# Kernel optimization log

Measured on AMD Instinct MI355X. Metric: run time of the kernel, lower is better.

## Reference

```python
import jax, jax.numpy as jnp
import numpy as np

N_NODES = 100000
N_EDGES = 3200000
D_FEAT = 128


def setup_inputs() -> dict:
    key = jax.random.key(0)
    k1, k2, k3, k4 = jax.random.split(key, 4)
    edge_row = jax.random.randint(k1, (N_EDGES,), 0, N_NODES, dtype=jnp.int64 if jax.config.jax_enable_x64 else jnp.int32)
    edge_col = jax.random.randint(k2, (N_EDGES,), 0, N_NODES, dtype=edge_row.dtype)
    edge_val = jax.random.uniform(k3, (N_EDGES,), dtype=jnp.float32)
    embeds = jax.random.normal(k4, (N_NODES, D_FEAT), dtype=jnp.float32)
    return {"edge_row": edge_row, "edge_col": edge_col, "edge_val": edge_val, "embeds": embeds}


def reference(edge_row, edge_col, edge_val, embeds):
    # SpMM: out[r] = sum_{e: row(e)=r} val(e) * embeds[col(e)]
    messages = edge_val[:, None] * embeds[edge_col]  # [E, D]
    out = jax.ops.segment_sum(messages, edge_row, num_segments=embeds.shape[0])  # [N, D]
    return out
```

## Files before the change

kernel.cpp:

```cpp
#include <hip/hip_runtime.h>
#include <stdint.h>

#define N_NODES 100000
#define D_FEAT  128
#define RSH     6
#define RPB     64
#define NBUCK   ((N_NODES + RPB - 1) / RPB)
#define CAPF    2304
#define KMAX    ((CAPF + 255) / 256)
#define OCAP    8192
#define SC_THR  1024
#define SC_EPT  8
#define SC_TILE (SC_THR * SC_EPT)
#define COLMASK 0x1FFFF

__global__ __launch_bounds__(SC_THR) void scatter_fixed_kernel(
    const int* __restrict__ row, const int* __restrict__ col,
    const float* __restrict__ val, int* __restrict__ cursor,
    int2* __restrict__ rec, int4* __restrict__ oflow, int* __restrict__ ocnt, int n,
    const uint64_t* __restrict__ embin, uint32_t* __restrict__ embbf, int do_conv)
{
    __shared__ int cnt[NBUCK];
    __shared__ int base[NBUCK];
    const int tid = threadIdx.x;

    if (do_conv) {
        const int n2 = N_NODES * (D_FEAT / 2);
        const int stride = (int)gridDim.x * SC_THR;
        for (int i = (int)blockIdx.x * SC_THR + tid; i < n2; i += stride) {
            uint64_t u = __builtin_nontemporal_load(embin + i);
            uint32_t bx = (uint32_t)u, by = (uint32_t)(u >> 32);
            bx = (bx + 0x7FFFu + ((bx >> 16) & 1u)) >> 16;
            by = (by + 0x7FFFu + ((by >> 16) & 1u)) >> 16;
            embbf[i] = bx | (by << 16);
        }
    }

    const int e0 = (int)blockIdx.x * SC_TILE + tid * SC_EPT;

    for (int i = tid; i < NBUCK; i += SC_THR) cnt[i] = 0;
    __syncthreads();

    int   r[SC_EPT], c[SC_EPT];
    float v[SC_EPT];
    if (e0 + SC_EPT <= n) {
        const int4* rp = (const int4*)(row + e0);
        const int4* cp = (const int4*)(col + e0);
        const float4* vp = (const float4*)(val + e0);
        #pragma unroll
        for (int q = 0; q < SC_EPT / 4; q++) {
            int4 rr = rp[q]; int4 cc = cp[q]; float4 vv = vp[q];
            r[q*4+0]=rr.x; r[q*4+1]=rr.y; r[q*4+2]=rr.z; r[q*4+3]=rr.w;
            c[q*4+0]=cc.x; c[q*4+1]=cc.y; c[q*4+2]=cc.z; c[q*4+3]=cc.w;
            v[q*4+0]=vv.x; v[q*4+1]=vv.y; v[q*4+2]=vv.z; v[q*4+3]=vv.w;
        }
    } else {
        #pragma unroll
        for (int k = 0; k < SC_EPT; k++) {
            int e = e0 + k;
            if (e < n) { r[k] = row[e]; c[k] = col[e]; v[k] = val[e]; }
            else       { r[k] = -1; }
        }
    }

    int rk[SC_EPT];
    #pragma unroll
    for (int k = 0; k < SC_EPT; k++)
        if (r[k] >= 0) rk[k] = atomicAdd(&cnt[r[k] >> RSH], 1);
    __syncthreads();

    for (int i = tid; i < NBUCK; i += SC_THR) {
        int cc = cnt[i];
        if (cc) base[i] = atomicAdd(&cursor[i], cc);
    }
    __syncthreads();

    #pragma unroll
    for (int k = 0; k < SC_EPT; k++) {
        if (r[k] >= 0) {
            int bk  = r[k] >> RSH;
            int pos = base[bk] + rk[k];
            if (pos < CAPF) {
                rec[(size_t)bk * CAPF + pos] =
                    make_int2(((r[k] & (RPB - 1)) << 17) | c[k], __float_as_int(v[k]));
            } else {
                int op = atomicAdd(ocnt, 1);
                if (op < OCAP) oflow[op] = make_int4(r[k], c[k], __float_as_int(v[k]), 0);
            }
        }
    }
}

template <bool BF16>
__global__ __launch_bounds__(256) void spmm_fixed_kernel(const int* __restrict__ fill,
                                                         const int2* __restrict__ rec,
                                                         const void* __restrict__ emb,
                                                         float* __restrict__ out)
{
    __shared__ int2 buf[CAPF];
    __shared__ int  cnt[RPB];
    __shared__ int  start[RPB];
    __shared__ int  sc_[RPB];

    const int tid  = threadIdx.x;
    const int lane = tid & 63;
    const int wv   = tid >> 6;
    const int b    = blockIdx.x;
    const int m    = min(fill[b], CAPF);
    const uint64_t* __restrict__ rec8 = (const uint64_t*)rec + (size_t)b * CAPF;
    const uint32_t* __restrict__ embu = (const uint32_t*)emb;
    const float2*   __restrict__ emb2 = (const float2*)emb;

    if (tid < RPB) cnt[tid] = 0;
    __syncthreads();

    int2 rc[KMAX];
    int  rk[KMAX];
    #pragma unroll
    for (int k = 0; k < KMAX; k++) {
        int i = k * 256 + tid;
        if (i < m) {
            uint64_t u = __builtin_nontemporal_load(rec8 + i);
            rc[k].x = (int)(uint32_t)u;
            rc[k].y = (int)(uint32_t)(u >> 32);
            rk[k] = atomicAdd(&cnt[(uint32_t)rc[k].x >> 17], 1);
        }
    }
    __syncthreads();
    if (tid < RPB) sc_[tid] = cnt[tid];
    __syncthreads();
    for (int off = 1; off < RPB; off <<= 1) {
        int t = 0;
        if (tid < RPB && tid >= off) t = sc_[tid - off];
        __syncthreads();
        if (tid < RPB) sc_[tid] += t;
        __syncthreads();
    }
    if (tid < RPB) start[tid] = sc_[tid] - cnt[tid];
    __syncthreads();
    #pragma unroll
    for (int k = 0; k < KMAX; k++) {
        int i = k * 256 + tid;
        if (i < m) buf[start[(uint32_t)rc[k].x >> 17] + rk[k]] = rc[k];
    }
    __syncthreads();

    for (int rl = wv * 16; rl < wv * 16 + 16; rl++) {
        const int s0 = start[rl];
        const int c0 = cnt[rl];
        float ax = 0.f, ay = 0.f;
        int j = 0;
        for (; j + 16 <= c0; j += 16) {
            uint32_t u[16]; float vv[16]; float2 m2[16];
            #pragma unroll
            for (int q = 0; q < 16; q++) {
                int2 e = buf[s0 + j + q];
                uint32_t off = (((uint32_t)e.x & COLMASK) << 6) | (uint32_t)lane;
                vv[q] = __int_as_float(e.y);
                if (BF16) u[q] = embu[off]; else m2[q] = emb2[off];
            }
            #pragma unroll
            for (int q = 0; q < 16; q++) {
                if (BF16) {
                    ax += vv[q] * __uint_as_float(u[q] << 16);
                    ay += vv[q] * __uint_as_float(u[q] & 0xFFFF0000u);
                } else {
                    ax += vv[q] * m2[q].x; ay += vv[q] * m2[q].y;
                }
            }
        }
        for (; j + 4 <= c0; j += 4) {
            uint32_t u[4]; float vv[4]; float2 m2[4];
            #pragma unroll
            for (int q = 0; q < 4; q++) {
                int2 e = buf[s0 + j + q];
                uint32_t off = (((uint32_t)e.x & COLMASK) << 6) | (uint32_t)lane;
                vv[q] = __int_as_float(e.y);
                if (BF16) u[q] = embu[off]; else m2[q] = emb2[off];
            }
            #pragma unroll
            for (int q = 0; q < 4; q++) {
                if (BF16) {
                    ax += vv[q] * __uint_as_float(u[q] << 16);
                    ay += vv[q] * __uint_as_float(u[q] & 0xFFFF0000u);
                } else {
                    ax += vv[q] * m2[q].x; ay += vv[q] * m2[q].y;
                }
            }
        }
        for (; j < c0; j++) {
            int2 e = buf[s0 + j];
            uint32_t off = (((uint32_t)e.x & COLMASK) << 6) | (uint32_t)lane;
            float vv = __int_as_float(e.y);
            if (BF16) {
                uint32_t u = embu[off];
                ax += vv * __uint_as_float(u << 16);
                ay += vv * __uint_as_float(u & 0xFFFF0000u);
            } else {
                float2 mm = emb2[off];
                ax += vv * mm.x; ay += vv * mm.y;
            }
        }
        const int grow = b * RPB + rl;
        if (grow < N_NODES) {
            uint64_t w = (uint64_t)__float_as_uint(ax) | ((uint64_t)__float_as_uint(ay) << 32);
            __builtin_nontemporal_store(w, (uint64_t*)out + (size_t)grow * 64 + lane);
        }
    }
}

__global__ __launch_bounds__(256) void oflow_kernel(const int4* __restrict__ oflow,
                                                    const int* __restrict__ ocnt,
                                                    const float* __restrict__ embeds,
                                                    float* __restrict__ out) {
    const int nof  = min(*ocnt, OCAP);
    const int lane = threadIdx.x & 63;
    const int w    = ((int)blockIdx.x * 256 + threadIdx.x) >> 6;
    const int nw   = ((int)gridDim.x * 256) >> 6;
    for (int i = w; i < nof; i += nw) {
        int4 e = oflow[i];
        const float2* src = (const float2*)(embeds + (size_t)e.y * D_FEAT);
        float2 mm = src[lane];
        float vv = __int_as_float(e.z);
        float* dst = out + (size_t)e.x * D_FEAT + (lane << 1);
        unsafeAtomicAdd(dst,     vv * mm.x);
        unsafeAtomicAdd(dst + 1, vv * mm.y);
    }
}

__global__ __launch_bounds__(256) void spmm_atomic_kernel(
    const int* __restrict__ edge_row, const int* __restrict__ edge_col,
    const float* __restrict__ edge_val, const float* __restrict__ embeds,
    float* __restrict__ out, int n_edges)
{
    const int lane    = threadIdx.x & 63;
    const int wave_id = ((int)blockIdx.x * blockDim.x + threadIdx.x) >> 6;
    const int n_waves = ((int)gridDim.x * blockDim.x) >> 6;
    for (int e = wave_id; e < n_edges; e += n_waves) {
        const int   r = edge_row[e];
        const int   c = edge_col[e];
        const float vv = edge_val[e];
        const float2* src = (const float2*)(embeds + (size_t)c * D_FEAT);
        float2 mm = src[lane];
        float* dst = out + (size_t)r * D_FEAT + (lane << 1);
        unsafeAtomicAdd(dst,     vv * mm.x);
        unsafeAtomicAdd(dst + 1, vv * mm.y);
    }
}

static inline size_t align256(size_t x) { return (x + 255) & ~(size_t)255; }

extern "C" void kernel_launch(void* const* d_in, const int* in_sizes, int n_in,
                              void* d_out, int out_size, void* d_ws, size_t ws_size,
                              hipStream_t stream) {
    const int*   edge_row = (const int*)d_in[0];
    const int*   edge_col = (const int*)d_in[1];
    const float* edge_val = (const float*)d_in[2];
    const float* embeds   = (const float*)d_in[3];
    float*       out      = (float*)d_out;

    const int n_edges = in_sizes[0];

    size_t off = 0;
    size_t o_cursor = off; off = align256(off + (size_t)(NBUCK + 1) * 4);
    size_t o_oflow  = off; off = align256(off + (size_t)OCAP * 16);
    size_t o_rec    = off; off = align256(off + (size_t)NBUCK * CAPF * 8);
    const size_t need_fp32 = off;
    size_t o_emb    = off; off = align256(off + (size_t)N_NODES * 64 * 4);
    const size_t need_bf16 = off;

    if (ws_size < need_fp32) {
        hipMemsetAsync(out, 0, (size_t)out_size * sizeof(float), stream);
        spmm_atomic_kernel<<<dim3(4096), dim3(256), 0, stream>>>(
            edge_row, edge_col, edge_val, embeds, out, n_edges);
        return;
    }

    char* ws = (char*)d_ws;
    int*      cursor = (int*)(ws + o_cursor);
    int*      ocnt   = cursor + NBUCK;
    int4*     oflow  = (int4*)(ws + o_oflow);
    int2*     rec    = (int2*)(ws + o_rec);
    uint32_t* embbf  = (uint32_t*)(ws + o_emb);

    const bool use_bf16 = (ws_size >= need_bf16);

    hipMemsetAsync(cursor, 0, (size_t)(NBUCK + 1) * 4, stream);
    scatter_fixed_kernel<<<dim3((n_edges + SC_TILE - 1) / SC_TILE), dim3(SC_THR), 0, stream>>>(
        edge_row, edge_col, edge_val, cursor, rec, oflow, ocnt, n_edges,
        (const uint64_t*)embeds, embbf, use_bf16 ? 1 : 0);
    if (use_bf16)
        spmm_fixed_kernel<true><<<dim3(NBUCK), dim3(256), 0, stream>>>(cursor, rec, embbf, out);
    else
        spmm_fixed_kernel<false><<<dim3(NBUCK), dim3(256), 0, stream>>>(cursor, rec, embeds, out);
    oflow_kernel<<<dim3(16), dim3(256), 0, stream>>>(oflow, ocnt, embeds, out);
}
```

Measured before the change: 275.4 us.

## Split each SpMM bucket across four blocks and batch gather loads

The SpMM kernel now launches four blocks per 64-row bucket. Each block re-reads the whole bucket's records but keeps only the 16 rows it owns, so each wave handles 4 rows instead of 16. This raises the number of blocks and waves in flight for better latency hiding, and adds launch_bounds occupancy hints and sched_barriers that group the 16 gather loads together. The cost is four times the record reads from global memory plus the extra local sorting work.

```diff
diff --git a/kernel.cpp b/kernel.cpp
--- a/kernel.cpp
+++ b/kernel.cpp
@@ -8,6 +8,7 @@
 #define NBUCK   ((N_NODES + RPB - 1) / RPB)
 #define CAPF    2304
 #define KMAX    ((CAPF + 255) / 256)
+#define QROWS   16
 #define OCAP    8192
 #define SC_THR  1024
 #define SC_EPT  8
@@ -92,26 +93,27 @@
 }
 
 template <bool BF16>
-__global__ __launch_bounds__(256) void spmm_fixed_kernel(const int* __restrict__ fill,
-                                                         const int2* __restrict__ rec,
-                                                         const void* __restrict__ emb,
-                                                         float* __restrict__ out)
+__global__ __launch_bounds__(256, 8) void spmm_fixed_kernel(const int* __restrict__ fill,
+                                                            const int2* __restrict__ rec,
+                                                            const void* __restrict__ emb,
+                                                            float* __restrict__ out)
 {
     __shared__ int2 buf[CAPF];
-    __shared__ int  cnt[RPB];
-    __shared__ int  start[RPB];
-    __shared__ int  sc_[RPB];
+    __shared__ int  cnt[QROWS];
+    __shared__ int  start[QROWS];
+    __shared__ int  sc_[QROWS];
 
     const int tid  = threadIdx.x;
     const int lane = tid & 63;
     const int wv   = tid >> 6;
-    const int b    = blockIdx.x;
+    const int b    = blockIdx.x >> 2;
+    const int qq   = blockIdx.x & 3;
     const int m    = min(fill[b], CAPF);
     const uint64_t* __restrict__ rec8 = (const uint64_t*)rec + (size_t)b * CAPF;
     const uint32_t* __restrict__ embu = (const uint32_t*)emb;
     const float2*   __restrict__ emb2 = (const float2*)emb;
 
-    if (tid < RPB) cnt[tid] = 0;
+    if (tid < QROWS) cnt[tid] = 0;
     __syncthreads();
 
     int2 rc[KMAX];
@@ -119,33 +121,36 @@
     #pragma unroll
     for (int k = 0; k < KMAX; k++) {
         int i = k * 256 + tid;
+        rk[k] = -1;
         if (i < m) {
             uint64_t u = __builtin_nontemporal_load(rec8 + i);
             rc[k].x = (int)(uint32_t)u;
             rc[k].y = (int)(uint32_t)(u >> 32);
-            rk[k] = atomicAdd(&cnt[(uint32_t)rc[k].x >> 17], 1);
-        }
-    }
-    __syncthreads();
-    if (tid < RPB) sc_[tid] = cnt[tid];
-    __syncthreads();
-    for (int off = 1; off < RPB; off <<= 1) {
+            int rl = (int)((uint32_t)rc[k].x >> 17);
+            if ((rl >> 4) == qq)
+                rk[k] = atomicAdd(&cnt[rl & (QROWS - 1)], 1);
+        }
+    }
+    __syncthreads();
+    if (tid < QROWS) sc_[tid] = cnt[tid];
+    __syncthreads();
+    for (int off = 1; off < QROWS; off <<= 1) {
         int t = 0;
-        if (tid < RPB && tid >= off) t = sc_[tid - off];
+        if (tid < QROWS && tid >= off) t = sc_[tid - off];
         __syncthreads();
-        if (tid < RPB) sc_[tid] += t;
+        if (tid < QROWS) sc_[tid] += t;
         __syncthreads();
     }
-    if (tid < RPB) start[tid] = sc_[tid] - cnt[tid];
+    if (tid < QROWS) start[tid] = sc_[tid] - cnt[tid];
     __syncthreads();
     #pragma unroll
     for (int k = 0; k < KMAX; k++) {
-        int i = k * 256 + tid;
-        if (i < m) buf[start[(uint32_t)rc[k].x >> 17] + rk[k]] = rc[k];
-    }
-    __syncthreads();
-
-    for (int rl = wv * 16; rl < wv * 16 + 16; rl++) {
+        if (rk[k] >= 0)
+            buf[start[((uint32_t)rc[k].x >> 17) & (QROWS - 1)] + rk[k]] = rc[k];
+    }
+    __syncthreads();
+
+    for (int rl = wv * 4; rl < wv * 4 + 4; rl++) {
         const int s0 = start[rl];
         const int c0 = cnt[rl];
         float ax = 0.f, ay = 0.f;
@@ -155,10 +160,16 @@
             #pragma unroll
             for (int q = 0; q < 16; q++) {
                 int2 e = buf[s0 + j + q];
-                uint32_t off = (((uint32_t)e.x & COLMASK) << 6) | (uint32_t)lane;
+                u[q]  = (((uint32_t)e.x & COLMASK) << 6) | (uint32_t)lane;
                 vv[q] = __int_as_float(e.y);
-                if (BF16) u[q] = embu[off]; else m2[q] = emb2[off];
-            }
+            }
+            __builtin_amdgcn_sched_barrier(0);
+            #pragma unroll
+            for (int q = 0; q < 16; q++) {
+                if (BF16) u[q] = embu[u[q]];
+                else      m2[q] = emb2[u[q]];
+            }
+            __builtin_amdgcn_sched_barrier(0);
             #pragma unroll
             for (int q = 0; q < 16; q++) {
                 if (BF16) {
@@ -174,9 +185,12 @@
             #pragma unroll
             for (int q = 0; q < 4; q++) {
                 int2 e = buf[s0 + j + q];
-                uint32_t off = (((uint32_t)e.x & COLMASK) << 6) | (uint32_t)lane;
+                u[q]  = (((uint32_t)e.x & COLMASK) << 6) | (uint32_t)lane;
                 vv[q] = __int_as_float(e.y);
-                if (BF16) u[q] = embu[off]; else m2[q] = emb2[off];
+            }
+            #pragma unroll
+            for (int q = 0; q < 4; q++) {
+                if (BF16) u[q] = embu[u[q]]; else m2[q] = emb2[u[q]];
             }
             #pragma unroll
             for (int q = 0; q < 4; q++) {
@@ -201,7 +215,7 @@
                 ax += vv * mm.x; ay += vv * mm.y;
             }
         }
-        const int grow = b * RPB + rl;
+        const int grow = b * RPB + qq * QROWS + rl;
         if (grow < N_NODES) {
             uint64_t w = (uint64_t)__float_as_uint(ax) | ((uint64_t)__float_as_uint(ay) << 32);
             __builtin_nontemporal_store(w, (uint64_t*)out + (size_t)grow * 64 + lane);
@@ -290,8 +304,8 @@
         edge_row, edge_col, edge_val, cursor, rec, oflow, ocnt, n_edges,
         (const uint64_t*)embeds, embbf, use_bf16 ? 1 : 0);
     if (use_bf16)
-        spmm_fixed_kernel<true><<<dim3(NBUCK), dim3(256), 0, stream>>>(cursor, rec, embbf, out);
+        spmm_fixed_kernel<true><<<dim3(NBUCK * 4), dim3(256), 0, stream>>>(cursor, rec, embbf, out);
     else
-        spmm_fixed_kernel<false><<<dim3(NBUCK), dim3(256), 0, stream>>>(cursor, rec, embeds, out);
+        spmm_fixed_kernel<false><<<dim3(NBUCK * 4), dim3(256), 0, stream>>>(cursor, rec, embeds, out);
     oflow_kernel<<<dim3(16), dim3(256), 0, stream>>>(oflow, ocnt, embeds, out);
 }
```

Result: no change. 280.1 us (+1.7%).

## Sort block edges by column slab then row to localize embedding gathers

Applied to the files above, without the earlier changes.

Within each row-bucket block, edges are now counting-sorted by a composite key of column slab (col>>13) and local row, so the block walks all rows one column slab at a time. Each wave keeps 16 row accumulators in registers and handles row pairs with up to 12 outstanding gathers. The aim is temporal locality across concurrent blocks in L2/MALL for the embedding table, plus more gathers in flight. The cost is a larger shared-memory prefix scan over 832 keys, more registers (launch_bounds hints 5 blocks/CU), and per-pair divergence overhead when there are few edges per key.

```diff
diff --git a/kernel.cpp b/kernel.cpp
--- a/kernel.cpp
+++ b/kernel.cpp
@@ -8,6 +8,8 @@
 #define NBUCK   ((N_NODES + RPB - 1) / RPB)
 #define CAPF    2304
 #define KMAX    ((CAPF + 255) / 256)
+#define NSH     13
+#define KEYS    (NSH * RPB)
 #define OCAP    8192
 #define SC_THR  1024
 #define SC_EPT  8
@@ -92,15 +94,15 @@
 }
 
 template <bool BF16>
-__global__ __launch_bounds__(256) void spmm_fixed_kernel(const int* __restrict__ fill,
-                                                         const int2* __restrict__ rec,
-                                                         const void* __restrict__ emb,
-                                                         float* __restrict__ out)
+__global__ __launch_bounds__(256, 5) void spmm_fixed_kernel(const int* __restrict__ fill,
+                                                            const int2* __restrict__ rec,
+                                                            const void* __restrict__ emb,
+                                                            float* __restrict__ out)
 {
     __shared__ int2 buf[CAPF];
-    __shared__ int  cnt[RPB];
-    __shared__ int  start[RPB];
-    __shared__ int  sc_[RPB];
+    __shared__ int  cnt[KEYS];
+    __shared__ int  start[KEYS];
+    __shared__ int  sc_[KEYS];
 
     const int tid  = threadIdx.x;
     const int lane = tid & 63;
@@ -111,99 +113,119 @@
     const uint32_t* __restrict__ embu = (const uint32_t*)emb;
     const float2*   __restrict__ emb2 = (const float2*)emb;
 
-    if (tid < RPB) cnt[tid] = 0;
+    for (int i = tid; i < KEYS; i += 256) cnt[i] = 0;
     __syncthreads();
 
     int2 rc[KMAX];
     int  rk[KMAX];
+    int  ky[KMAX];
     #pragma unroll
     for (int k = 0; k < KMAX; k++) {
         int i = k * 256 + tid;
+        rk[k] = -1;
         if (i < m) {
             uint64_t u = __builtin_nontemporal_load(rec8 + i);
             rc[k].x = (int)(uint32_t)u;
             rc[k].y = (int)(uint32_t)(u >> 32);
-            rk[k] = atomicAdd(&cnt[(uint32_t)rc[k].x >> 17], 1);
-        }
-    }
-    __syncthreads();
-    if (tid < RPB) sc_[tid] = cnt[tid];
-    __syncthreads();
-    for (int off = 1; off < RPB; off <<= 1) {
-        int t = 0;
-        if (tid < RPB && tid >= off) t = sc_[tid - off];
+            uint32_t col = (uint32_t)rc[k].x & COLMASK;
+            uint32_t rl  = (uint32_t)rc[k].x >> 17;
+            ky[k] = (int)((col >> 13) * RPB + rl);
+            rk[k] = atomicAdd(&cnt[ky[k]], 1);
+        }
+    }
+    __syncthreads();
+
+    for (int i = tid; i < KEYS; i += 256) sc_[i] = cnt[i];
+    __syncthreads();
+    for (int off = 1; off < KEYS; off <<= 1) {
+        int t[4];
+        #pragma unroll
+        for (int z = 0; z < 4; z++) {
+            int i = tid + z * 256;
+            t[z] = (i < KEYS && i >= off) ? sc_[i - off] : 0;
+        }
         __syncthreads();
-        if (tid < RPB) sc_[tid] += t;
+        #pragma unroll
+        for (int z = 0; z < 4; z++) {
+            int i = tid + z * 256;
+            if (i < KEYS) sc_[i] += t[z];
+        }
         __syncthreads();
     }
-    if (tid < RPB) start[tid] = sc_[tid] - cnt[tid];
-    __syncthreads();
-    #pragma unroll
-    for (int k = 0; k < KMAX; k++) {
-        int i = k * 256 + tid;
-        if (i < m) buf[start[(uint32_t)rc[k].x >> 17] + rk[k]] = rc[k];
-    }
-    __syncthreads();
-
-    for (int rl = wv * 16; rl < wv * 16 + 16; rl++) {
-        const int s0 = start[rl];
-        const int c0 = cnt[rl];
-        float ax = 0.f, ay = 0.f;
-        int j = 0;
-        for (; j + 16 <= c0; j += 16) {
-            uint32_t u[16]; float vv[16]; float2 m2[16];
+    for (int i = tid; i < KEYS; i += 256) start[i] = sc_[i] - cnt[i];
+    __syncthreads();
+
+    #pragma unroll
+    for (int k = 0; k < KMAX; k++)
+        if (rk[k] >= 0) buf[start[ky[k]] + rk[k]] = rc[k];
+    __syncthreads();
+
+    float ax[16], ay[16];
+    #pragma unroll
+    for (int p = 0; p < 16; p++) { ax[p] = 0.f; ay[p] = 0.f; }
+
+    for (int s = 0; s < NSH; s++) {
+        const int kbase = s * RPB + wv * 16;
+        #pragma unroll
+        for (int p = 0; p < 8; p++) {
+            const int ka = kbase + 2 * p;
+            const int ca = cnt[ka], cb = cnt[ka + 1];
+            const int nfull = __builtin_amdgcn_readfirstlane(ca + cb);
+            if (nfull == 0) continue;
+            const int ss = __builtin_amdgcn_readfirstlane(ca);
+            const int sa = start[ka];
+            const int nn = nfull < 12 ? nfull : 12;
+
+            uint32_t u[12]; float vv[12]; float2 m2[12];
             #pragma unroll
-            for (int q = 0; q < 16; q++) {
-                int2 e = buf[s0 + j + q];
+            for (int q = 0; q < 12; q++) {
+                if (q < nn) {
+                    int2 e = buf[sa + q];
+                    u[q]  = (((uint32_t)e.x & COLMASK) << 6) | (uint32_t)lane;
+                    vv[q] = __int_as_float(e.y);
+                }
+            }
+            #pragma unroll
+            for (int q = 0; q < 12; q++) {
+                if (q < nn) { if (BF16) u[q] = embu[u[q]]; else m2[q] = emb2[u[q]]; }
+            }
+            #pragma unroll
+            for (int q = 0; q < 12; q++) {
+                if (q >= nn) break;
+                float tx, ty;
+                if (BF16) {
+                    tx = vv[q] * __uint_as_float(u[q] << 16);
+                    ty = vv[q] * __uint_as_float(u[q] & 0xFFFF0000u);
+                } else {
+                    tx = vv[q] * m2[q].x; ty = vv[q] * m2[q].y;
+                }
+                if (q < ss) { ax[2*p]   += tx; ay[2*p]   += ty; }
+                else        { ax[2*p+1] += tx; ay[2*p+1] += ty; }
+            }
+            for (int j = 12; j < nfull; j++) {
+                int2 e = buf[sa + j];
                 uint32_t off = (((uint32_t)e.x & COLMASK) << 6) | (uint32_t)lane;
-                vv[q] = __int_as_float(e.y);
-                if (BF16) u[q] = embu[off]; else m2[q] = emb2[off];
-            }
-            #pragma unroll
-            for (int q = 0; q < 16; q++) {
+                float vj = __int_as_float(e.y);
+                float tx, ty;
                 if (BF16) {
-                    ax += vv[q] * __uint_as_float(u[q] << 16);
-                    ay += vv[q] * __uint_as_float(u[q] & 0xFFFF0000u);
+                    uint32_t w = embu[off];
+                    tx = vj * __uint_as_float(w << 16);
+                    ty = vj * __uint_as_float(w & 0xFFFF0000u);
                 } else {
-                    ax += vv[q] * m2[q].x; ay += vv[q] * m2[q].y;
+                    float2 mm = emb2[off];
+                    tx = vj * mm.x; ty = vj * mm.y;
                 }
-            }
-        }
-        for (; j + 4 <= c0; j += 4) {
-            uint32_t u[4]; float vv[4]; float2 m2[4];
-            #pragma unroll
-            for (int q = 0; q < 4; q++) {
-                int2 e = buf[s0 + j + q];
-                uint32_t off = (((uint32_t)e.x & COLMASK) << 6) | (uint32_t)lane;
-                vv[q] = __int_as_float(e.y);
-                if (BF16) u[q] = embu[off]; else m2[q] = emb2[off];
-            }
-            #pragma unroll
-            for (int q = 0; q < 4; q++) {
-                if (BF16) {
-                    ax += vv[q] * __uint_as_float(u[q] << 16);
-                    ay += vv[q] * __uint_as_float(u[q] & 0xFFFF0000u);
-                } else {
-                    ax += vv[q] * m2[q].x; ay += vv[q] * m2[q].y;
-                }
-            }
-        }
-        for (; j < c0; j++) {
-            int2 e = buf[s0 + j];
-            uint32_t off = (((uint32_t)e.x & COLMASK) << 6) | (uint32_t)lane;
-            float vv = __int_as_float(e.y);
-            if (BF16) {
-                uint32_t u = embu[off];
-                ax += vv * __uint_as_float(u << 16);
-                ay += vv * __uint_as_float(u & 0xFFFF0000u);
-            } else {
-                float2 mm = emb2[off];
-                ax += vv * mm.x; ay += vv * mm.y;
-            }
-        }
-        const int grow = b * RPB + rl;
+                if (j < ss) { ax[2*p]   += tx; ay[2*p]   += ty; }
+                else        { ax[2*p+1] += tx; ay[2*p+1] += ty; }
+            }
+        }
+    }
+
+    #pragma unroll
+    for (int p = 0; p < 16; p++) {
+        const int grow = b * RPB + wv * 16 + p;
         if (grow < N_NODES) {
-            uint64_t w = (uint64_t)__float_as_uint(ax) | ((uint64_t)__float_as_uint(ay) << 32);
+            uint64_t w = (uint64_t)__float_as_uint(ax[p]) | ((uint64_t)__float_as_uint(ay[p]) << 32);
             __builtin_nontemporal_store(w, (uint64_t*)out + (size_t)grow * 64 + lane);
         }
     }
```

New measurement: 569.5 us. 107% more time.

## Halve rows per bucket, pad bucket cursors, batch gather loads, raise occupancy

Applied to the files above, without the earlier changes.

Buckets now cover 32 rows with half the per-bucket capacity, so there are twice as many spmm blocks and shared memory per block is halved. The launch bound asks for 8 blocks per SM to raise occupancy. Bucket cursors are spaced 16 ints apart when workspace allows, to cut atomic contention and false sharing on cache lines. The gather loop computes all addresses before issuing the loads, so more memory requests are in flight. The bounds check on output rows is removed; 100000 divides evenly by 32, so it is safe for this size. Smaller per-bucket capacity may push more edges onto the atomic overflow path.

```diff
diff --git a/kernel.cpp b/kernel.cpp
--- a/kernel.cpp
+++ b/kernel.cpp
@@ -3,10 +3,10 @@
 
 #define N_NODES 100000
 #define D_FEAT  128
-#define RSH     6
-#define RPB     64
+#define RSH     5
+#define RPB     32
 #define NBUCK   ((N_NODES + RPB - 1) / RPB)
-#define CAPF    2304
+#define CAPF    1152
 #define KMAX    ((CAPF + 255) / 256)
 #define OCAP    8192
 #define SC_THR  1024
@@ -18,7 +18,8 @@
     const int* __restrict__ row, const int* __restrict__ col,
     const float* __restrict__ val, int* __restrict__ cursor,
     int2* __restrict__ rec, int4* __restrict__ oflow, int* __restrict__ ocnt, int n,
-    const uint64_t* __restrict__ embin, uint32_t* __restrict__ embbf, int do_conv)
+    const uint64_t* __restrict__ embin, uint32_t* __restrict__ embbf, int do_conv,
+    int cpad)
 {
     __shared__ int cnt[NBUCK];
     __shared__ int base[NBUCK];
@@ -71,7 +72,7 @@
 
     for (int i = tid; i < NBUCK; i += SC_THR) {
         int cc = cnt[i];
-        if (cc) base[i] = atomicAdd(&cursor[i], cc);
+        if (cc) base[i] = atomicAdd(&cursor[(size_t)i * cpad], cc);
     }
     __syncthreads();
 
@@ -92,10 +93,11 @@
 }
 
 template <bool BF16>
-__global__ __launch_bounds__(256) void spmm_fixed_kernel(const int* __restrict__ fill,
-                                                         const int2* __restrict__ rec,
-                                                         const void* __restrict__ emb,
-                                                         float* __restrict__ out)
+__global__ __launch_bounds__(256, 8) void spmm_fixed_kernel(const int* __restrict__ fill,
+                                                            const int2* __restrict__ rec,
+                                                            const void* __restrict__ emb,
+                                                            float* __restrict__ out,
+                                                            int cpad)
 {
     __shared__ int2 buf[CAPF];
     __shared__ int  cnt[RPB];
@@ -106,7 +108,7 @@
     const int lane = tid & 63;
     const int wv   = tid >> 6;
     const int b    = blockIdx.x;
-    const int m    = min(fill[b], CAPF);
+    const int m    = min(fill[(size_t)b * cpad], CAPF);
     const uint64_t* __restrict__ rec8 = (const uint64_t*)rec + (size_t)b * CAPF;
     const uint32_t* __restrict__ embu = (const uint32_t*)emb;
     const float2*   __restrict__ emb2 = (const float2*)emb;
@@ -145,7 +147,7 @@
     }
     __syncthreads();
 
-    for (int rl = wv * 16; rl < wv * 16 + 16; rl++) {
+    for (int rl = wv * 8; rl < wv * 8 + 8; rl++) {
         const int s0 = start[rl];
         const int c0 = cnt[rl];
         float ax = 0.f, ay = 0.f;
@@ -155,9 +157,12 @@
             #pragma unroll
             for (int q = 0; q < 16; q++) {
                 int2 e = buf[s0 + j + q];
-                uint32_t off = (((uint32_t)e.x & COLMASK) << 6) | (uint32_t)lane;
+                u[q]  = (((uint32_t)e.x & COLMASK) << 6) | (uint32_t)lane;
                 vv[q] = __int_as_float(e.y);
-                if (BF16) u[q] = embu[off]; else m2[q] = emb2[off];
+            }
+            #pragma unroll
+            for (int q = 0; q < 16; q++) {
+                if (BF16) u[q] = embu[u[q]]; else m2[q] = emb2[u[q]];
             }
             #pragma unroll
             for (int q = 0; q < 16; q++) {
@@ -174,9 +179,12 @@
             #pragma unroll
             for (int q = 0; q < 4; q++) {
                 int2 e = buf[s0 + j + q];
-                uint32_t off = (((uint32_t)e.x & COLMASK) << 6) | (uint32_t)lane;
+                u[q]  = (((uint32_t)e.x & COLMASK) << 6) | (uint32_t)lane;
                 vv[q] = __int_as_float(e.y);
-                if (BF16) u[q] = embu[off]; else m2[q] = emb2[off];
+            }
+            #pragma unroll
+            for (int q = 0; q < 4; q++) {
+                if (BF16) u[q] = embu[u[q]]; else m2[q] = emb2[u[q]];
             }
             #pragma unroll
             for (int q = 0; q < 4; q++) {
@@ -202,10 +210,8 @@
             }
         }
         const int grow = b * RPB + rl;
-        if (grow < N_NODES) {
-            uint64_t w = (uint64_t)__float_as_uint(ax) | ((uint64_t)__float_as_uint(ay) << 32);
-            __builtin_nontemporal_store(w, (uint64_t*)out + (size_t)grow * 64 + lane);
-        }
+        uint64_t w = (uint64_t)__float_as_uint(ax) | ((uint64_t)__float_as_uint(ay) << 32);
+        __builtin_nontemporal_store(w, (uint64_t*)out + (size_t)grow * 64 + lane);
     }
 }
 
@@ -261,15 +267,19 @@
 
     const int n_edges = in_sizes[0];
 
-    size_t off = 0;
-    size_t o_cursor = off; off = align256(off + (size_t)(NBUCK + 1) * 4);
-    size_t o_oflow  = off; off = align256(off + (size_t)OCAP * 16);
-    size_t o_rec    = off; off = align256(off + (size_t)NBUCK * CAPF * 8);
-    const size_t need_fp32 = off;
-    size_t o_emb    = off; off = align256(off + (size_t)N_NODES * 64 * 4);
-    const size_t need_bf16 = off;
-
-    if (ws_size < need_fp32) {
+    const size_t cur16  = align256(((size_t)NBUCK * 16 + 16) * 4);
+    const size_t cur1   = align256(((size_t)NBUCK + 16) * 4);
+    const size_t of_sz  = align256((size_t)OCAP * 16);
+    const size_t rec_sz = align256((size_t)NBUCK * CAPF * 8);
+    const size_t emb_sz = align256((size_t)N_NODES * 64 * 4);
+
+    int  cpad;
+    bool use_bf16;
+    size_t cur_sz;
+    if (ws_size >= cur16 + of_sz + rec_sz + emb_sz)      { cpad = 16; use_bf16 = true;  cur_sz = cur16; }
+    else if (ws_size >= cur1 + of_sz + rec_sz + emb_sz)  { cpad = 1;  use_bf16 = true;  cur_sz = cur1;  }
+    else if (ws_size >= cur1 + of_sz + rec_sz)           { cpad = 1;  use_bf16 = false; cur_sz = cur1;  }
+    else {
         hipMemsetAsync(out, 0, (size_t)out_size * sizeof(float), stream);
         spmm_atomic_kernel<<<dim3(4096), dim3(256), 0, stream>>>(
             edge_row, edge_col, edge_val, embeds, out, n_edges);
@@ -277,21 +287,19 @@
     }
 
     char* ws = (char*)d_ws;
-    int*      cursor = (int*)(ws + o_cursor);
-    int*      ocnt   = cursor + NBUCK;
-    int4*     oflow  = (int4*)(ws + o_oflow);
-    int2*     rec    = (int2*)(ws + o_rec);
-    uint32_t* embbf  = (uint32_t*)(ws + o_emb);
-
-    const bool use_bf16 = (ws_size >= need_bf16);
-
-    hipMemsetAsync(cursor, 0, (size_t)(NBUCK + 1) * 4, stream);
+    int*      cursor = (int*)ws;
+    int*      ocnt   = cursor + (size_t)NBUCK * cpad;
+    int4*     oflow  = (int4*)(ws + cur_sz);
+    int2*     rec    = (int2*)(ws + cur_sz + of_sz);
+    uint32_t* embbf  = (uint32_t*)(ws + cur_sz + of_sz + rec_sz);
+
+    hipMemsetAsync(cursor, 0, ((size_t)NBUCK * cpad + 1) * 4, stream);
     scatter_fixed_kernel<<<dim3((n_edges + SC_TILE - 1) / SC_TILE), dim3(SC_THR), 0, stream>>>(
         edge_row, edge_col, edge_val, cursor, rec, oflow, ocnt, n_edges,
-        (const uint64_t*)embeds, embbf, use_bf16 ? 1 : 0);
+        (const uint64_t*)embeds, embbf, use_bf16 ? 1 : 0, cpad);
     if (use_bf16)
-        spmm_fixed_kernel<true><<<dim3(NBUCK), dim3(256), 0, stream>>>(cursor, rec, embbf, out);
+        spmm_fixed_kernel<true><<<dim3(NBUCK), dim3(256), 0, stream>>>(cursor, rec, embbf, out, cpad);
     else
-        spmm_fixed_kernel<false><<<dim3(NBUCK), dim3(256), 0, stream>>>(cursor, rec, embeds, out);
+        spmm_fixed_kernel<false><<<dim3(NBUCK), dim3(256), 0, stream>>>(cursor, rec, embeds, out, cpad);
     oflow_kernel<<<dim3(16), dim3(256), 0, stream>>>(oflow, ocnt, embeds, out);
 }
```

Result: slower. 308.3 us (+12.0%).
